# Kernel optimization log

Hardware: AMD Instinct MI355X
Metric: run time of the kernel (lower is better)

## Reference

```python
import jax, jax.numpy as jnp
import numpy as np

NUM_HEADS = 12
H = W = 64            # spatial grid (SAM ViT-B global attention)
DIM = 768
HEAD_DIM = DIM // NUM_HEADS


def setup_inputs() -> dict:
    key = jax.random.key(0)
    ks = jax.random.split(key, 7)
    return {
        "x": jax.random.normal(ks[0], (1, H, W, DIM), dtype=jnp.float32),
        "qkv_w": jax.random.normal(ks[1], (3 * DIM, DIM), dtype=jnp.float32) * 0.02,
        "qkv_b": jax.random.normal(ks[2], (3 * DIM,), dtype=jnp.float32) * 0.02,
        "proj_w": jax.random.normal(ks[3], (DIM, DIM), dtype=jnp.float32) * 0.02,
        "proj_b": jax.random.normal(ks[4], (DIM,), dtype=jnp.float32) * 0.02,
        "rel_pos_h": jax.random.normal(ks[5], (2 * H - 1, HEAD_DIM), dtype=jnp.float32) * 0.02,
        "rel_pos_w": jax.random.normal(ks[6], (2 * W - 1, HEAD_DIM), dtype=jnp.float32) * 0.02,
    }


def _get_rel_pos(size: int, rel_pos: jnp.ndarray) -> jnp.ndarray:
    # q_size == k_size == size; rel_pos already has length 2*size-1 (no interp).
    coords = jnp.arange(size)[:, None] - jnp.arange(size)[None, :] + (size - 1)
    return rel_pos[coords]  # [size, size, head_dim]


def reference(x, qkv_w, qkv_b, proj_w, proj_b, rel_pos_h, rel_pos_w):
    B, h, w, C = x.shape
    nh, hd = NUM_HEADS, C // NUM_HEADS
    S = h * w
    scale = hd ** -0.5

    qkv = x.reshape(B, S, C) @ qkv_w.T + qkv_b            # [B, S, 3C]
    qkv = qkv.reshape(B, S, 3, nh, hd).transpose(2, 0, 3, 1, 4)
    qkv = qkv.reshape(3, B * nh, S, hd)
    q, k, v = qkv[0], qkv[1], qkv[2]                      # [B*nh, S, hd]

    attn = jnp.einsum('bqc,bkc->bqk', q * scale, k)       # [B*nh, S, S]

    Rh = _get_rel_pos(h, rel_pos_h)                       # [h, h, hd]
    Rw = _get_rel_pos(w, rel_pos_w)                       # [w, w, hd]
    r_q = q.reshape(B * nh, h, w, hd)
    rel_h = jnp.einsum('bhwc,hkc->bhwk', r_q, Rh)         # [B*nh, h, w, h]
    rel_w = jnp.einsum('bhwc,wkc->bhwk', r_q, Rw)         # [B*nh, h, w, w]
    attn = (attn.reshape(B * nh, h, w, h, w)
            + rel_h[:, :, :, :, None]
            + rel_w[:, :, :, None, :]).reshape(B * nh, S, S)

    attn = jax.nn.softmax(attn, axis=-1)
    out = jnp.einsum('bqk,bkc->bqc', attn, v)             # [B*nh, S, hd]
    out = out.reshape(B, nh, h, w, hd).transpose(0, 2, 3, 1, 4).reshape(B, h, w, C)
    return out @ proj_w.T + proj_b
```

## Files before the change

kernel.cpp:

```cpp
#include <hip/hip_runtime.h>


typedef __bf16 bf16;
typedef __bf16 bf16x8 __attribute__((ext_vector_type(8)));
typedef __bf16 bf16x4 __attribute__((ext_vector_type(4)));
typedef float f32x4 __attribute__((ext_vector_type(4)));
typedef float f32x16 __attribute__((ext_vector_type(16)));
typedef unsigned int u32;

__device__ __forceinline__ f32x4 mfma16(bf16x8 a, bf16x8 b, f32x4 c) {
  return __builtin_amdgcn_mfma_f32_16x16x32_bf16(a, b, c, 0, 0, 0);
}
__device__ __forceinline__ f32x16 mfma32(bf16x8 a, bf16x8 b, f32x16 c) {
  return __builtin_amdgcn_mfma_f32_32x32x16_bf16(a, b, c, 0, 0, 0);
}

typedef const __attribute__((address_space(1))) void* gas_ptr;
typedef __attribute__((address_space(3))) void* las_ptr;
__device__ __forceinline__ void gl_lds16(const void* g, void* l) {
  __builtin_amdgcn_global_load_lds((gas_ptr)g, (las_ptr)l, 16, 0, 0);
}

#if defined(__has_builtin)
#if __has_builtin(__builtin_amdgcn_permlane32_swap)
#define HAVE_PLSWAP 1
#endif
#endif
__device__ __forceinline__ void pswap_u(u32& a, u32& b) {
#ifdef HAVE_PLSWAP
  auto r = __builtin_amdgcn_permlane32_swap(a, b, false, false);
  a = r[0]; b = r[1];
#else
  const bool hi = (threadIdx.x & 32) != 0;
  u32 sa = (u32)__shfl_xor((int)a, 32, 64);
  u32 sb = (u32)__shfl_xor((int)b, 32, 64);
  u32 na = hi ? sb : a;
  u32 nb = hi ? b : sa;
  a = na; b = nb;
#endif
}
__device__ __forceinline__ void pswap_f(float& a, float& b) {
  u32 x = __float_as_uint(a), y = __float_as_uint(b);
  pswap_u(x, y);
  a = __uint_as_float(x); b = __uint_as_float(y);
}

#define L2E 1.4426950408889634f
#define SCK 0.18033688011112042f

__global__ __launch_bounds__(256) void cvt3(
    const float* __restrict__ a, bf16* __restrict__ oa,
    const float* __restrict__ b, bf16* __restrict__ ob,
    const float* __restrict__ c, bf16* __restrict__ oc) {
  int blk = blockIdx.x;
  const float* src;
  bf16* dst;
  int base;
  if (blk < 1536)       { src = a; dst = oa; base = blk; }
  else if (blk < 2400)  { src = b; dst = ob; base = blk - 1536; }
  else                  { src = c; dst = oc; base = blk - 2400; }
  int idx = (base * 256 + threadIdx.x) * 8;
  f32x4 x = *(const f32x4*)&src[idx];
  f32x4 y = *(const f32x4*)&src[idx + 4];
  bf16x8 o;
#pragma unroll
  for (int j = 0; j < 4; j++) { o[j] = (bf16)x[j]; o[j + 4] = (bf16)y[j]; }
  *(bf16x8*)&dst[idx] = o;
}

template <int MODE>
__global__ __launch_bounds__(256) void gemm128(
    const bf16* __restrict__ A, const bf16* __restrict__ B,
    const float* __restrict__ bias, int K, int N,
    bf16* __restrict__ q_s, bf16* __restrict__ k_f, bf16* __restrict__ v_f,
    float* __restrict__ outf) {
  __shared__ __align__(16) bf16 lA[128 * 64];
  __shared__ __align__(16) bf16 lB[128 * 64];
  const int tid = threadIdx.x;
  const int w = tid >> 6, l = tid & 63;
  const int nbx = gridDim.x;
  const int flat = blockIdx.y * nbx + blockIdx.x;
  const int nwg = nbx * gridDim.y;
  const int idx = (flat & 7) * (nwg >> 3) + (flat >> 3);
  const int n0 = (idx % nbx) * 128, m0 = (idx / nbx) * 128;

  f32x4 acc[4][4] = {};

  int rowc[4], sloc[4];
#pragma unroll
  for (int j = 0; j < 4; j++) {
    const int c = w * 4 + j;
    rowc[j] = c * 8 + (l >> 3);
    sloc[j] = (((l & 7) ^ (l >> 3) ^ c) & 7) * 8;
  }
  const int mw = (w & 1) * 64, nw = (w >> 1) * 64;

  for (int k0 = 0; k0 < K; k0 += 64) {
    __syncthreads();
#pragma unroll
    for (int j = 0; j < 4; j++) {
      gl_lds16(&A[(size_t)(m0 + rowc[j]) * K + k0 + sloc[j]],
               (char*)lA + (w * 4 + j) * 1024);
      gl_lds16(&B[(size_t)(n0 + rowc[j]) * K + k0 + sloc[j]],
               (char*)lB + (w * 4 + j) * 1024);
    }
    __syncthreads();
    bf16x8 af[2][4], bfr[2][4];
#pragma unroll
    for (int ks = 0; ks < 2; ks++)
#pragma unroll
      for (int i = 0; i < 4; i++) {
        const int rA = mw + i * 16 + (l & 15);
        const int rB = nw + i * 16 + (l & 15);
        const int slot = ks * 4 + (l >> 4);
        const int fA = ((rA ^ (rA >> 3)) & 7), fB = ((rB ^ (rB >> 3)) & 7);
        af[ks][i] = *(const bf16x8*)((const char*)lA + rA * 128 + ((slot ^ fA) & 7) * 16);
        bfr[ks][i] = *(const bf16x8*)((const char*)lB + rB * 128 + ((slot ^ fB) & 7) * 16);
      }
#pragma unroll
    for (int ks = 0; ks < 2; ks++)
#pragma unroll
      for (int mi = 0; mi < 4; mi++)
#pragma unroll
        for (int ni = 0; ni < 4; ni++)
          acc[mi][ni] = mfma16(af[ks][mi], bfr[ks][ni], acc[mi][ni]);
  }

  if (MODE == 0 && n0 >= 1536) {
    bf16* Lt = lA;
#pragma unroll 1
    for (int pass = 0; pass < 2; ++pass) {
      __syncthreads();
      if ((w >> 1) == pass) {
        char* R = (char*)Lt + (w & 1) * 8192;
#pragma unroll
        for (int ni = 0; ni < 4; ni++) {
          const float bv = bias[n0 + nw + ni * 16 + (l & 15)];
          const int nl = ni * 16 + (l & 15);
#pragma unroll
          for (int mi = 0; mi < 4; mi++)
#pragma unroll
            for (int i2 = 0; i2 < 2; i2++) {
              const int ml2 = (mi * 16 + (l >> 4) * 4 + i2 * 2) * 2;
              union { bf16 b[2]; u32 u; } pk;
              pk.b[0] = (bf16)(acc[mi][ni][i2 * 2] + bv);
              pk.b[1] = (bf16)(acc[mi][ni][i2 * 2 + 1] + bv);
              *(u32*)(R + nl * 128 + (ml2 ^ ((nl & 7) << 4))) = pk.u;
            }
        }
      }
      __syncthreads();
      if ((w >> 1) == pass) {
        const char* R = (const char*)Lt + (w & 1) * 8192;
#pragma unroll
        for (int r = 0; r < 8; r++) {
          const int nl = r * 8 + (l >> 3);
          const int pc = ((l & 7) * 16) ^ ((nl & 7) << 4);
          bf16x8 val = *(const bf16x8*)(R + nl * 128 + pc);
          const int n = n0 + pass * 64 + nl;
          const int head = (n - 1536) >> 6, hd = n & 63;
          const int mg = m0 + (w & 1) * 64 + (l & 7) * 8;
          const int t = mg >> 6, kh2 = (mg >> 5) & 1;
          const int st = (mg >> 4) & 1, hh = (mg >> 3) & 1;
          const size_t vidx =
              ((((((size_t)head * 64 + t) * 2 + kh2) * 2 + st) * 2 + hh) * 64 +
               hd) * 8;
          *(bf16x8*)&v_f[vidx] = val;
        }
      }
    }
    return;
  }

#pragma unroll
  for (int ni = 0; ni < 4; ni++) {
    const int n = n0 + nw + ni * 16 + (l & 15);
    const float bv = bias[n];
#pragma unroll
    for (int mi = 0; mi < 4; mi++) {
#pragma unroll
      for (int i = 0; i < 4; i++) {
        const int m = m0 + mw + mi * 16 + (l >> 4) * 4 + i;
        const float v = acc[mi][ni][i] + bv;
        if (MODE == 0) {
          const int which = n / 768, hn = n % 768;
          const int head = hn >> 6, hd = hn & 63;
          if (which == 0) {
            q_s[((size_t)head * 4096 + m) * 64 + hd] = (bf16)v;
          } else {
            const int t = m >> 6, kh2 = (m >> 5) & 1, r5 = m & 31;
            const int s = hd >> 4, h = (hd >> 3) & 1, j = hd & 7;
            const size_t kidx =
                ((((((size_t)head * 64 + t) * 2 + kh2) * 4 + s) * 2 + h) * 32 +
                 r5) * 8 + j;
            k_f[kidx] = (bf16)(v * SCK);
          }
        } else {
          outf[(size_t)m * N + n] = v;
        }
      }
    }
  }
}

__global__ __launch_bounds__(64) void rel_pos_w(
    const bf16* __restrict__ q_s, const float* __restrict__ table,
    float* __restrict__ out) {
  const int l = threadIdx.x;
  const int p = blockIdx.x, head = blockIdx.y;
  const size_t hbase = (size_t)head * 4096 * 64;

  f32x4 acc[4][4] = {};
#pragma unroll
  for (int ks = 0; ks < 2; ks++) {
    bf16x8 af[4], bfr[4];
#pragma unroll
    for (int mi = 0; mi < 4; mi++) {
      const int row = mi * 16 + (l & 15);
      const int s = row * 64 + p;
      af[mi] = *(const bf16x8*)&q_s[hbase + (size_t)s * 64 + ks * 32 + (l >> 4) * 8];
    }
#pragma unroll
    for (int ni = 0; ni < 4; ni++) {
      const int col = ni * 16 + (l & 15);
      const float* tp = &table[(size_t)(p - col + 63) * 64 + ks * 32 + (l >> 4) * 8];
      f32x4 t0 = *(const f32x4*)tp;
      f32x4 t1 = *(const f32x4*)(tp + 4);
      bf16x8 bb;
#pragma unroll
      for (int j = 0; j < 4; j++) { bb[j] = (bf16)t0[j]; bb[j + 4] = (bf16)t1[j]; }
      bfr[ni] = bb;
    }
#pragma unroll
    for (int mi = 0; mi < 4; mi++)
#pragma unroll
      for (int ni = 0; ni < 4; ni++)
        acc[mi][ni] = mfma16(af[mi], bfr[ni], acc[mi][ni]);
  }
#pragma unroll
  for (int mi = 0; mi < 4; mi++)
#pragma unroll
    for (int ni = 0; ni < 4; ni++)
#pragma unroll
      for (int i = 0; i < 4; i++) {
        const int row = mi * 16 + (l >> 4) * 4 + i;
        const int col = ni * 16 + (l & 15);
        const int sq = row * 64 + p;
        out[hbase + (size_t)sq * 64 + col] = acc[mi][ni][i];
      }
}

__global__ __launch_bounds__(256, 3) void flash_attn(
    const bf16* __restrict__ q_s, const bf16* __restrict__ k_f,
    const bf16* __restrict__ v_f, const float* __restrict__ rph,
    const float* __restrict__ bias_w, bf16* __restrict__ attn_out) {
  __shared__ __align__(16) char smem[16896];
  float* lBH = (float*)smem;

  const int tid = threadIdx.x;
  const int w = tid >> 6, l = tid & 63;
  const int r5 = l & 31, h = l >> 5;
  const int qg = w & 1, kh2 = w >> 1;
  const int f = blockIdx.x;
  const int g = (f & 7) * 96 + (f >> 3);
  const int head = g >> 6, qh = g & 63;
  const size_t hbase = (size_t)head << 18;
  const int qloc = qg * 32 + r5;
  const size_t sq = (size_t)qh * 64 + qloc;

  {
    const int q16 = l & 15, g4 = l >> 4;
    const size_t sq16 = (size_t)qh * 64 + w * 16 + q16;
    bf16x8 qf16[2];
    qf16[0] = *(const bf16x8*)&q_s[hbase + sq16 * 64 + g4 * 8];
    qf16[1] = *(const bf16x8*)&q_s[hbase + sq16 * 64 + 32 + g4 * 8];
    f32x4 abh[4] = {};
#pragma unroll
    for (int ks = 0; ks < 2; ks++)
#pragma unroll
      for (int ni = 0; ni < 4; ni++) {
        const int kh = ni * 16 + q16;
        const float* tp = &rph[(size_t)(qh + 63 - kh) * 64 + ks * 32 + g4 * 8];
        f32x4 t0 = *(const f32x4*)tp;
        f32x4 t1 = *(const f32x4*)(tp + 4);
        bf16x8 rf;
#pragma unroll
        for (int j = 0; j < 4; j++) { rf[j] = (bf16)t0[j]; rf[j + 4] = (bf16)t1[j]; }
        abh[ni] = mfma16(rf, qf16[ks], abh[ni]);
      }
#pragma unroll
    for (int ni = 0; ni < 4; ni++)
#pragma unroll
      for (int i = 0; i < 4; i++)
        lBH[(w * 16 + q16) * 65 + ni * 16 + g4 * 4 + i] = abh[ni][i] * L2E;
  }

  bf16x8 qv[4];
#pragma unroll
  for (int s = 0; s < 4; s++)
    qv[s] = *(const bf16x8*)&q_s[hbase + sq * 64 + s * 16 + h * 8];

  f32x16 c2v;
#pragma unroll
  for (int G = 0; G < 4; G++) {
    f32x4 cv = *(const f32x4*)&bias_w[hbase + sq * 64 + kh2 * 32 + G * 8 + h * 4];
#pragma unroll
    for (int i = 0; i < 4; i++) c2v[G * 4 + i] = cv[i] * L2E;
  }

  const bf16* kp = k_f + hbase + kh2 * 2048 + h * 256 + r5 * 8;
  const bf16* vp = v_f + hbase + kh2 * 2048 + h * 512 + r5 * 8;
  const float* lbhp = lBH + qloc * 65;

  f32x16 o[2] = {};
  float mrun = -1e30f, lrun = 0.f;

  __syncthreads();

  for (int t = 0; t < 64; t++) {
    f32x16 sacc = c2v;
    __builtin_amdgcn_s_setprio(1);
#pragma unroll
    for (int s = 0; s < 4; s++) {
      bf16x8 kf = *(const bf16x8*)((const char*)kp + s * 1024);
      sacc = mfma32(kf, qv[s], sacc);
    }
    __builtin_amdgcn_s_setprio(0);

    float pm = fmaxf(
        fmaxf(fmaxf(fmaxf(sacc[0], sacc[1]), sacc[2]),
              fmaxf(fmaxf(sacc[3], sacc[4]), sacc[5])),
        fmaxf(fmaxf(fmaxf(sacc[6], sacc[7]), fmaxf(sacc[8], sacc[9])),
              fmaxf(fmaxf(sacc[10], fmaxf(sacc[11], sacc[12])),
                    fmaxf(sacc[13], fmaxf(sacc[14], sacc[15])))));
    { float t2 = pm; pswap_f(t2, pm); pm = fmaxf(t2, pm); }
    const float bh2 = lbhp[t];
    const float rmf = pm + bh2;

    if (!__all(rmf - mrun <= 8.f)) {
      const float mn = fmaxf(mrun, rmf);
      const float al = __builtin_amdgcn_exp2f(mrun - mn);
      mrun = mn;
      lrun *= al;
      o[0] *= al;
      o[1] *= al;
    }

    const float d = bh2 - mrun;
    float rs = 0.f;
    u32 w8[8];
#pragma unroll
    for (int j = 0; j < 8; j++) {
      float e0 = __builtin_amdgcn_exp2f(sacc[2 * j] + d);
      float e1 = __builtin_amdgcn_exp2f(sacc[2 * j + 1] + d);
      rs += e0 + e1;
      union { bf16 b[2]; u32 u; } cvu;
      cvu.b[0] = (bf16)e0;
      cvu.b[1] = (bf16)e1;
      w8[j] = cvu.u;
    }
    { float t2 = rs; pswap_f(t2, rs); rs = t2 + rs; }
    lrun += rs;

#pragma unroll
    for (int st = 0; st < 2; st++) {
      union { u32 u[4]; bf16x8 v; } pf;
      u32 a0 = w8[4 * st], b0 = w8[4 * st + 2];
      u32 a1 = w8[4 * st + 1], b1 = w8[4 * st + 3];
      pswap_u(a0, b0);
      pswap_u(a1, b1);
      pf.u[0] = a0; pf.u[1] = a1; pf.u[2] = b0; pf.u[3] = b1;
      __builtin_amdgcn_s_setprio(1);
#pragma unroll
      for (int T = 0; T < 2; T++) {
        bf16x8 vf = *(const bf16x8*)((const char*)vp + st * 2048 + T * 512);
        o[T] = mfma32(vf, pf.v, o[T]);
      }
      __builtin_amdgcn_s_setprio(0);
    }

    kp += 4096;
    vp += 4096;
  }

  __syncthreads();

  float* MM = (float*)smem;
  float* ML = (float*)(smem + 256);
  float* MO = (float*)(smem + 512);
  if (w >= 2) {
    if (h == 0) { MM[qg * 32 + r5] = mrun; ML[qg * 32 + r5] = lrun; }
#pragma unroll
    for (int T = 0; T < 2; T++)
#pragma unroll
      for (int G = 0; G < 4; G++) {
        f32x4 ov;
#pragma unroll
        for (int i = 0; i < 4; i++) ov[i] = o[T][4 * G + i];
        *(f32x4*)&MO[qg * 2048 + r5 * 64 + T * 32 + G * 8 + h * 4] = ov;
      }
  }
  __syncthreads();
  if (w < 2) {
    const float mp = MM[qg * 32 + r5], lp = ML[qg * 32 + r5];
    const float mT = fmaxf(mrun, mp);
    const float a = __builtin_amdgcn_exp2f(mrun - mT);
    const float b = __builtin_amdgcn_exp2f(mp - mT);
    const float inv = 1.f / (lrun * a + lp * b);
#pragma unroll
    for (int T = 0; T < 2; T++)
#pragma unroll
      for (int G = 0; G < 4; G++) {
        f32x4 po = *(const f32x4*)&MO[qg * 2048 + r5 * 64 + T * 32 + G * 8 + h * 4];
        bf16x4 ob;
#pragma unroll
        for (int i = 0; i < 4; i++)
          ob[i] = (bf16)((o[T][4 * G + i] * a + po[i] * b) * inv);
        *(bf16x4*)&attn_out[sq * 768 + head * 64 + T * 32 + G * 8 + h * 4] = ob;
      }
  }
}

extern "C" void kernel_launch(void* const* d_in, const int* in_sizes, int n_in,
                              void* d_out, int out_size, void* d_ws, size_t ws_size,
                              hipStream_t stream) {
  const float* x      = (const float*)d_in[0];
  const float* qkv_w  = (const float*)d_in[1];
  const float* qkv_b  = (const float*)d_in[2];
  const float* proj_w = (const float*)d_in[3];
  const float* proj_b = (const float*)d_in[4];
  const float* rph    = (const float*)d_in[5];
  const float* rpw    = (const float*)d_in[6];

  char* ws = (char*)d_ws;
  bf16*  xb    = (bf16*)(ws);
  bf16*  wqkv  = (bf16*)(ws + 6291456);
  bf16*  wproj = (bf16*)(ws + 9830400);
  bf16*  q_s   = (bf16*)(ws + 11010048);
  bf16*  k_f   = (bf16*)(ws + 17301504);
  bf16*  v_f   = (bf16*)(ws + 23592960);
  bf16*  attno = (bf16*)(ws + 29884416);
  float* bwv   = (float*)(ws + 36175872);

  cvt3<<<2688, 256, 0, stream>>>(x, xb, qkv_w, wqkv, proj_w, wproj);

  gemm128<0><<<dim3(18, 32), 256, 0, stream>>>(xb, wqkv, qkv_b, 768, 2304,
                                               q_s, k_f, v_f, nullptr);

  rel_pos_w<<<dim3(64, 12), 64, 0, stream>>>(q_s, rpw, bwv);

  flash_attn<<<768, 256, 0, stream>>>(q_s, k_f, v_f, rph, bwv, attno);

  gemm128<1><<<dim3(6, 32), 256, 0, stream>>>(attno, wproj, proj_b, 768, 768,
                                              nullptr, nullptr, nullptr,
                                              (float*)d_out);
}
```

Measured before the change: 257.3 us.

## Software-pipeline K/V register loads in flash attention and pre-convert rel-pos tables

The flash attention main loop is unrolled by two and double-buffers the K fragments in registers, loading the next tile's K and the current V before the current tile's compute so global latency overlaps the MFMA and softmax work. Separately, the rel_pos_h and rel_pos_w tables are converted to bf16 once in the cvt kernel, so the rel-pos and attention kernels read bf16 directly instead of loading fp32 and converting per use. The extra live registers from double buffering may raise register pressure under the 3-blocks-per-SM launch bound and risk spills.

```diff
diff --git a/kernel.cpp b/kernel.cpp
--- a/kernel.cpp
+++ b/kernel.cpp
@@ -51,15 +51,20 @@
 __global__ __launch_bounds__(256) void cvt3(
     const float* __restrict__ a, bf16* __restrict__ oa,
     const float* __restrict__ b, bf16* __restrict__ ob,
-    const float* __restrict__ c, bf16* __restrict__ oc) {
+    const float* __restrict__ c, bf16* __restrict__ oc,
+    const float* __restrict__ t1, bf16* __restrict__ ot1,
+    const float* __restrict__ t2, bf16* __restrict__ ot2) {
   int blk = blockIdx.x;
   const float* src;
   bf16* dst;
-  int base;
-  if (blk < 1536)       { src = a; dst = oa; base = blk; }
-  else if (blk < 2400)  { src = b; dst = ob; base = blk - 1536; }
-  else                  { src = c; dst = oc; base = blk - 2400; }
+  int base, lim;
+  if (blk < 1536)       { src = a;  dst = oa;  base = blk;        lim = 3145728; }
+  else if (blk < 2400)  { src = b;  dst = ob;  base = blk - 1536; lim = 1769472; }
+  else if (blk < 2688)  { src = c;  dst = oc;  base = blk - 2400; lim = 589824; }
+  else if (blk < 2692)  { src = t1; dst = ot1; base = blk - 2688; lim = 8128; }
+  else                  { src = t2; dst = ot2; base = blk - 2692; lim = 8128; }
   int idx = (base * 256 + threadIdx.x) * 8;
+  if (idx >= lim) return;
   f32x4 x = *(const f32x4*)&src[idx];
   f32x4 y = *(const f32x4*)&src[idx + 4];
   bf16x8 o;
@@ -204,7 +209,7 @@
 }
 
 __global__ __launch_bounds__(64) void rel_pos_w(
-    const bf16* __restrict__ q_s, const float* __restrict__ table,
+    const bf16* __restrict__ q_s, const bf16* __restrict__ rpw_b,
     float* __restrict__ out) {
   const int l = threadIdx.x;
   const int p = blockIdx.x, head = blockIdx.y;
@@ -223,13 +228,8 @@
 #pragma unroll
     for (int ni = 0; ni < 4; ni++) {
       const int col = ni * 16 + (l & 15);
-      const float* tp = &table[(size_t)(p - col + 63) * 64 + ks * 32 + (l >> 4) * 8];
-      f32x4 t0 = *(const f32x4*)tp;
-      f32x4 t1 = *(const f32x4*)(tp + 4);
-      bf16x8 bb;
-#pragma unroll
-      for (int j = 0; j < 4; j++) { bb[j] = (bf16)t0[j]; bb[j + 4] = (bf16)t1[j]; }
-      bfr[ni] = bb;
+      bfr[ni] = *(const bf16x8*)&rpw_b[(size_t)(p - col + 63) * 64 + ks * 32 +
+                                       (l >> 4) * 8];
     }
 #pragma unroll
     for (int mi = 0; mi < 4; mi++)
@@ -252,7 +252,7 @@
 
 __global__ __launch_bounds__(256, 3) void flash_attn(
     const bf16* __restrict__ q_s, const bf16* __restrict__ k_f,
-    const bf16* __restrict__ v_f, const float* __restrict__ rph,
+    const bf16* __restrict__ v_f, const bf16* __restrict__ rph_b,
     const float* __restrict__ bias_w, bf16* __restrict__ attn_out) {
   __shared__ __align__(16) char smem[16896];
   float* lBH = (float*)smem;
@@ -280,12 +280,8 @@
 #pragma unroll
       for (int ni = 0; ni < 4; ni++) {
         const int kh = ni * 16 + q16;
-        const float* tp = &rph[(size_t)(qh + 63 - kh) * 64 + ks * 32 + g4 * 8];
-        f32x4 t0 = *(const f32x4*)tp;
-        f32x4 t1 = *(const f32x4*)(tp + 4);
-        bf16x8 rf;
-#pragma unroll
-        for (int j = 0; j < 4; j++) { rf[j] = (bf16)t0[j]; rf[j + 4] = (bf16)t1[j]; }
+        bf16x8 rf = *(const bf16x8*)&rph_b[(size_t)(qh + 63 - kh) * 64 +
+                                           ks * 32 + g4 * 8];
         abh[ni] = mfma16(rf, qf16[ks], abh[ni]);
       }
 #pragma unroll
@@ -315,73 +311,96 @@
   f32x16 o[2] = {};
   float mrun = -1e30f, lrun = 0.f;
 
+  bf16x8 kA0 = *(const bf16x8*)(kp);
+  bf16x8 kA1 = *(const bf16x8*)(kp + 512);
+  bf16x8 kA2 = *(const bf16x8*)(kp + 1024);
+  bf16x8 kA3 = *(const bf16x8*)(kp + 1536);
+  kp += 4096;
+  bf16x8 kB0, kB1, kB2, kB3, v0, v1, v2, v3;
+
+#define COMP(K0, K1, K2, K3, t)                                              \
+  do {                                                                       \
+    f32x16 sacc = c2v;                                                       \
+    __builtin_amdgcn_s_setprio(1);                                           \
+    sacc = mfma32(K0, qv[0], sacc);                                          \
+    sacc = mfma32(K1, qv[1], sacc);                                          \
+    sacc = mfma32(K2, qv[2], sacc);                                          \
+    sacc = mfma32(K3, qv[3], sacc);                                          \
+    __builtin_amdgcn_s_setprio(0);                                           \
+    float pm = fmaxf(                                                        \
+        fmaxf(fmaxf(fmaxf(sacc[0], sacc[1]), sacc[2]),                       \
+              fmaxf(fmaxf(sacc[3], sacc[4]), sacc[5])),                      \
+        fmaxf(fmaxf(fmaxf(sacc[6], sacc[7]), fmaxf(sacc[8], sacc[9])),       \
+              fmaxf(fmaxf(sacc[10], fmaxf(sacc[11], sacc[12])),              \
+                    fmaxf(sacc[13], fmaxf(sacc[14], sacc[15])))));           \
+    { float t2_ = pm; pswap_f(t2_, pm); pm = fmaxf(t2_, pm); }               \
+    const float bh2 = lbhp[(t)];                                             \
+    const float rmf = pm + bh2;                                              \
+    if (!__all(rmf - mrun <= 8.f)) {                                         \
+      const float mn = fmaxf(mrun, rmf);                                     \
+      const float al = __builtin_amdgcn_exp2f(mrun - mn);                    \
+      mrun = mn;                                                             \
+      lrun *= al;                                                            \
+      o[0] *= al;                                                            \
+      o[1] *= al;                                                            \
+    }                                                                        \
+    const float d = bh2 - mrun;                                              \
+    float rs = 0.f;                                                          \
+    u32 w8[8];                                                               \
+    _Pragma("unroll")                                                        \
+    for (int j = 0; j < 8; j++) {                                            \
+      float e0 = __builtin_amdgcn_exp2f(sacc[2 * j] + d);                    \
+      float e1 = __builtin_amdgcn_exp2f(sacc[2 * j + 1] + d);                \
+      rs += e0 + e1;                                                         \
+      union { bf16 b[2]; u32 u; } cvu;                                       \
+      cvu.b[0] = (bf16)e0;                                                   \
+      cvu.b[1] = (bf16)e1;                                                   \
+      w8[j] = cvu.u;                                                         \
+    }                                                                        \
+    { float t2_ = rs; pswap_f(t2_, rs); rs = t2_ + rs; }                     \
+    lrun += rs;                                                              \
+    _Pragma("unroll")                                                        \
+    for (int st = 0; st < 2; st++) {                                         \
+      union { u32 u[4]; bf16x8 v; } pf;                                      \
+      u32 a0 = w8[4 * st], b0 = w8[4 * st + 2];                              \
+      u32 a1 = w8[4 * st + 1], b1 = w8[4 * st + 3];                          \
+      pswap_u(a0, b0);                                                       \
+      pswap_u(a1, b1);                                                       \
+      pf.u[0] = a0; pf.u[1] = a1; pf.u[2] = b0; pf.u[3] = b1;                \
+      __builtin_amdgcn_s_setprio(1);                                         \
+      o[0] = mfma32(st ? v2 : v0, pf.v, o[0]);                               \
+      o[1] = mfma32(st ? v3 : v1, pf.v, o[1]);                               \
+      __builtin_amdgcn_s_setprio(0);                                         \
+    }                                                                        \
+  } while (0)
+
   __syncthreads();
 
-  for (int t = 0; t < 64; t++) {
-    f32x16 sacc = c2v;
-    __builtin_amdgcn_s_setprio(1);
-#pragma unroll
-    for (int s = 0; s < 4; s++) {
-      bf16x8 kf = *(const bf16x8*)((const char*)kp + s * 1024);
-      sacc = mfma32(kf, qv[s], sacc);
-    }
-    __builtin_amdgcn_s_setprio(0);
-
-    float pm = fmaxf(
-        fmaxf(fmaxf(fmaxf(sacc[0], sacc[1]), sacc[2]),
-              fmaxf(fmaxf(sacc[3], sacc[4]), sacc[5])),
-        fmaxf(fmaxf(fmaxf(sacc[6], sacc[7]), fmaxf(sacc[8], sacc[9])),
-              fmaxf(fmaxf(sacc[10], fmaxf(sacc[11], sacc[12])),
-                    fmaxf(sacc[13], fmaxf(sacc[14], sacc[15])))));
-    { float t2 = pm; pswap_f(t2, pm); pm = fmaxf(t2, pm); }
-    const float bh2 = lbhp[t];
-    const float rmf = pm + bh2;
-
-    if (!__all(rmf - mrun <= 8.f)) {
-      const float mn = fmaxf(mrun, rmf);
-      const float al = __builtin_amdgcn_exp2f(mrun - mn);
-      mrun = mn;
-      lrun *= al;
-      o[0] *= al;
-      o[1] *= al;
-    }
-
-    const float d = bh2 - mrun;
-    float rs = 0.f;
-    u32 w8[8];
-#pragma unroll
-    for (int j = 0; j < 8; j++) {
-      float e0 = __builtin_amdgcn_exp2f(sacc[2 * j] + d);
-      float e1 = __builtin_amdgcn_exp2f(sacc[2 * j + 1] + d);
-      rs += e0 + e1;
-      union { bf16 b[2]; u32 u; } cvu;
-      cvu.b[0] = (bf16)e0;
-      cvu.b[1] = (bf16)e1;
-      w8[j] = cvu.u;
-    }
-    { float t2 = rs; pswap_f(t2, rs); rs = t2 + rs; }
-    lrun += rs;
-
-#pragma unroll
-    for (int st = 0; st < 2; st++) {
-      union { u32 u[4]; bf16x8 v; } pf;
-      u32 a0 = w8[4 * st], b0 = w8[4 * st + 2];
-      u32 a1 = w8[4 * st + 1], b1 = w8[4 * st + 3];
-      pswap_u(a0, b0);
-      pswap_u(a1, b1);
-      pf.u[0] = a0; pf.u[1] = a1; pf.u[2] = b0; pf.u[3] = b1;
-      __builtin_amdgcn_s_setprio(1);
-#pragma unroll
-      for (int T = 0; T < 2; T++) {
-        bf16x8 vf = *(const bf16x8*)((const char*)vp + st * 2048 + T * 512);
-        o[T] = mfma32(vf, pf.v, o[T]);
-      }
-      __builtin_amdgcn_s_setprio(0);
-    }
-
+  for (int t = 0; t < 64; t += 2) {
+    v0 = *(const bf16x8*)(vp);
+    v1 = *(const bf16x8*)(vp + 256);
+    v2 = *(const bf16x8*)(vp + 1024);
+    v3 = *(const bf16x8*)(vp + 1280);
+    kB0 = *(const bf16x8*)(kp);
+    kB1 = *(const bf16x8*)(kp + 512);
+    kB2 = *(const bf16x8*)(kp + 1024);
+    kB3 = *(const bf16x8*)(kp + 1536);
     kp += 4096;
     vp += 4096;
-  }
+    COMP(kA0, kA1, kA2, kA3, t);
+    v0 = *(const bf16x8*)(vp);
+    v1 = *(const bf16x8*)(vp + 256);
+    v2 = *(const bf16x8*)(vp + 1024);
+    v3 = *(const bf16x8*)(vp + 1280);
+    kA0 = *(const bf16x8*)(kp);
+    kA1 = *(const bf16x8*)(kp + 512);
+    kA2 = *(const bf16x8*)(kp + 1024);
+    kA3 = *(const bf16x8*)(kp + 1536);
+    kp += 4096;
+    vp += 4096;
+    COMP(kB0, kB1, kB2, kB3, t + 1);
+  }
+#undef COMP
 
   __syncthreads();
 
@@ -441,15 +460,18 @@
   bf16*  v_f   = (bf16*)(ws + 23592960);
   bf16*  attno = (bf16*)(ws + 29884416);
   float* bwv   = (float*)(ws + 36175872);
-
-  cvt3<<<2688, 256, 0, stream>>>(x, xb, qkv_w, wqkv, proj_w, wproj);
+  bf16*  rph_b = (bf16*)(ws + 48758784);
+  bf16*  rpw_b = (bf16*)(ws + 48775040);
+
+  cvt3<<<2696, 256, 0, stream>>>(x, xb, qkv_w, wqkv, proj_w, wproj,
+                                 rph, rph_b, rpw, rpw_b);
 
   gemm128<0><<<dim3(18, 32), 256, 0, stream>>>(xb, wqkv, qkv_b, 768, 2304,
                                                q_s, k_f, v_f, nullptr);
 
-  rel_pos_w<<<dim3(64, 12), 64, 0, stream>>>(q_s, rpw, bwv);
-
-  flash_attn<<<768, 256, 0, stream>>>(q_s, k_f, v_f, rph, bwv, attno);
+  rel_pos_w<<<dim3(64, 12), 64, 0, stream>>>(q_s, rpw_b, bwv);
+
+  flash_attn<<<768, 256, 0, stream>>>(q_s, k_f, v_f, rph_b, bwv, attno);
 
   gemm128<1><<<dim3(6, 32), 256, 0, stream>>>(attno, wproj, proj_b, 768, 768,
                                               nullptr, nullptr, nullptr,
```

New measurement: 247.8 us. -3.7%, faster.

## Split flash attention key loop across 8 waves and pre-convert rel-pos tables

Applied to the files above, without the earlier changes.

The flash attention kernel now runs 512 threads per block, so each query group's 64 key tiles are split four ways (two kh2 halves times two interleaved tiles) instead of two. The per-block merge becomes a 4-way log-sum-exp combine through larger shared memory. K and V fragments are also loaded at the top of each iteration ahead of the MFMAs to hide latency. The rel-pos tables are converted to bf16 once in the cvt kernel and rel_pos_w packs 4 positions per block. The cost is more LDS (51KB), a heavier reduction, and possibly lower occupancy.

```diff
diff --git a/kernel.cpp b/kernel.cpp
--- a/kernel.cpp
+++ b/kernel.cpp
@@ -51,15 +51,20 @@
 __global__ __launch_bounds__(256) void cvt3(
     const float* __restrict__ a, bf16* __restrict__ oa,
     const float* __restrict__ b, bf16* __restrict__ ob,
-    const float* __restrict__ c, bf16* __restrict__ oc) {
+    const float* __restrict__ c, bf16* __restrict__ oc,
+    const float* __restrict__ t1, bf16* __restrict__ ot1,
+    const float* __restrict__ t2, bf16* __restrict__ ot2) {
   int blk = blockIdx.x;
   const float* src;
   bf16* dst;
-  int base;
-  if (blk < 1536)       { src = a; dst = oa; base = blk; }
-  else if (blk < 2400)  { src = b; dst = ob; base = blk - 1536; }
-  else                  { src = c; dst = oc; base = blk - 2400; }
+  int base, lim;
+  if (blk < 1536)       { src = a;  dst = oa;  base = blk;        lim = 3145728; }
+  else if (blk < 2400)  { src = b;  dst = ob;  base = blk - 1536; lim = 1769472; }
+  else if (blk < 2688)  { src = c;  dst = oc;  base = blk - 2400; lim = 589824; }
+  else if (blk < 2692)  { src = t1; dst = ot1; base = blk - 2688; lim = 8128; }
+  else                  { src = t2; dst = ot2; base = blk - 2692; lim = 8128; }
   int idx = (base * 256 + threadIdx.x) * 8;
+  if (idx >= lim) return;
   f32x4 x = *(const f32x4*)&src[idx];
   f32x4 y = *(const f32x4*)&src[idx + 4];
   bf16x8 o;
@@ -203,11 +208,12 @@
   }
 }
 
-__global__ __launch_bounds__(64) void rel_pos_w(
-    const bf16* __restrict__ q_s, const float* __restrict__ table,
+__global__ __launch_bounds__(256) void rel_pos_w(
+    const bf16* __restrict__ q_s, const bf16* __restrict__ rpw_b,
     float* __restrict__ out) {
-  const int l = threadIdx.x;
-  const int p = blockIdx.x, head = blockIdx.y;
+  const int l = threadIdx.x & 63;
+  const int p = blockIdx.x * 4 + (threadIdx.x >> 6);
+  const int head = blockIdx.y;
   const size_t hbase = (size_t)head * 4096 * 64;
 
   f32x4 acc[4][4] = {};
@@ -223,13 +229,8 @@
 #pragma unroll
     for (int ni = 0; ni < 4; ni++) {
       const int col = ni * 16 + (l & 15);
-      const float* tp = &table[(size_t)(p - col + 63) * 64 + ks * 32 + (l >> 4) * 8];
-      f32x4 t0 = *(const f32x4*)tp;
-      f32x4 t1 = *(const f32x4*)(tp + 4);
-      bf16x8 bb;
-#pragma unroll
-      for (int j = 0; j < 4; j++) { bb[j] = (bf16)t0[j]; bb[j + 4] = (bf16)t1[j]; }
-      bfr[ni] = bb;
+      bfr[ni] = *(const bf16x8*)&rpw_b[(size_t)(p - col + 63) * 64 + ks * 32 +
+                                       (l >> 4) * 8];
     }
 #pragma unroll
     for (int mi = 0; mi < 4; mi++)
@@ -250,17 +251,17 @@
       }
 }
 
-__global__ __launch_bounds__(256, 3) void flash_attn(
+__global__ __launch_bounds__(512, 4) void flash_attn(
     const bf16* __restrict__ q_s, const bf16* __restrict__ k_f,
-    const bf16* __restrict__ v_f, const float* __restrict__ rph,
+    const bf16* __restrict__ v_f, const bf16* __restrict__ rph_b,
     const float* __restrict__ bias_w, bf16* __restrict__ attn_out) {
-  __shared__ __align__(16) char smem[16896];
+  __shared__ __align__(16) char smem[51200];
   float* lBH = (float*)smem;
 
   const int tid = threadIdx.x;
   const int w = tid >> 6, l = tid & 63;
   const int r5 = l & 31, h = l >> 5;
-  const int qg = w & 1, kh2 = w >> 1;
+  const int kh2 = w & 1, tp = (w >> 1) & 1, qg = w >> 2;
   const int f = blockIdx.x;
   const int g = (f & 7) * 96 + (f >> 3);
   const int head = g >> 6, qh = g & 63;
@@ -268,7 +269,7 @@
   const int qloc = qg * 32 + r5;
   const size_t sq = (size_t)qh * 64 + qloc;
 
-  {
+  if (w < 4) {
     const int q16 = l & 15, g4 = l >> 4;
     const size_t sq16 = (size_t)qh * 64 + w * 16 + q16;
     bf16x8 qf16[2];
@@ -280,12 +281,8 @@
 #pragma unroll
       for (int ni = 0; ni < 4; ni++) {
         const int kh = ni * 16 + q16;
-        const float* tp = &rph[(size_t)(qh + 63 - kh) * 64 + ks * 32 + g4 * 8];
-        f32x4 t0 = *(const f32x4*)tp;
-        f32x4 t1 = *(const f32x4*)(tp + 4);
-        bf16x8 rf;
-#pragma unroll
-        for (int j = 0; j < 4; j++) { rf[j] = (bf16)t0[j]; rf[j + 4] = (bf16)t1[j]; }
+        bf16x8 rf = *(const bf16x8*)&rph_b[(size_t)(qh + 63 - kh) * 64 +
+                                           ks * 32 + g4 * 8];
         abh[ni] = mfma16(rf, qf16[ks], abh[ni]);
       }
 #pragma unroll
@@ -308,23 +305,33 @@
     for (int i = 0; i < 4; i++) c2v[G * 4 + i] = cv[i] * L2E;
   }
 
-  const bf16* kp = k_f + hbase + kh2 * 2048 + h * 256 + r5 * 8;
-  const bf16* vp = v_f + hbase + kh2 * 2048 + h * 512 + r5 * 8;
-  const float* lbhp = lBH + qloc * 65;
+  const bf16* kp = k_f + hbase + tp * 4096 + kh2 * 2048 + h * 256 + r5 * 8;
+  const bf16* vp = v_f + hbase + tp * 4096 + kh2 * 2048 + h * 512 + r5 * 8;
+  const float* lbhp = lBH + qloc * 65 + tp;
 
   f32x16 o[2] = {};
   float mrun = -1e30f, lrun = 0.f;
 
   __syncthreads();
 
-  for (int t = 0; t < 64; t++) {
+  for (int i = 0; i < 32; i++) {
+    bf16x8 k0 = *(const bf16x8*)(kp);
+    bf16x8 k1 = *(const bf16x8*)(kp + 512);
+    bf16x8 k2 = *(const bf16x8*)(kp + 1024);
+    bf16x8 k3 = *(const bf16x8*)(kp + 1536);
+    bf16x8 v0 = *(const bf16x8*)(vp);
+    bf16x8 v1 = *(const bf16x8*)(vp + 256);
+    bf16x8 v2 = *(const bf16x8*)(vp + 1024);
+    bf16x8 v3 = *(const bf16x8*)(vp + 1280);
+    kp += 8192;
+    vp += 8192;
+
     f32x16 sacc = c2v;
     __builtin_amdgcn_s_setprio(1);
-#pragma unroll
-    for (int s = 0; s < 4; s++) {
-      bf16x8 kf = *(const bf16x8*)((const char*)kp + s * 1024);
-      sacc = mfma32(kf, qv[s], sacc);
-    }
+    sacc = mfma32(k0, qv[0], sacc);
+    sacc = mfma32(k1, qv[1], sacc);
+    sacc = mfma32(k2, qv[2], sacc);
+    sacc = mfma32(k3, qv[3], sacc);
     __builtin_amdgcn_s_setprio(0);
 
     float pm = fmaxf(
@@ -334,7 +341,7 @@
               fmaxf(fmaxf(sacc[10], fmaxf(sacc[11], sacc[12])),
                     fmaxf(sacc[13], fmaxf(sacc[14], sacc[15])))));
     { float t2 = pm; pswap_f(t2, pm); pm = fmaxf(t2, pm); }
-    const float bh2 = lbhp[t];
+    const float bh2 = lbhp[2 * i];
     const float rmf = pm + bh2;
 
     if (!__all(rmf - mrun <= 8.f)) {
@@ -371,25 +378,23 @@
       pswap_u(a1, b1);
       pf.u[0] = a0; pf.u[1] = a1; pf.u[2] = b0; pf.u[3] = b1;
       __builtin_amdgcn_s_setprio(1);
-#pragma unroll
-      for (int T = 0; T < 2; T++) {
-        bf16x8 vf = *(const bf16x8*)((const char*)vp + st * 2048 + T * 512);
-        o[T] = mfma32(vf, pf.v, o[T]);
-      }
+      o[0] = mfma32(st ? v2 : v0, pf.v, o[0]);
+      o[1] = mfma32(st ? v3 : v1, pf.v, o[1]);
       __builtin_amdgcn_s_setprio(0);
     }
-
-    kp += 4096;
-    vp += 4096;
   }
 
   __syncthreads();
 
   float* MM = (float*)smem;
-  float* ML = (float*)(smem + 256);
-  float* MO = (float*)(smem + 512);
-  if (w >= 2) {
-    if (h == 0) { MM[qg * 32 + r5] = mrun; ML[qg * 32 + r5] = lrun; }
+  float* ML = (float*)(smem + 1024);
+  float* MO = (float*)(smem + 2048);
+  const int slot = (w & 3) - 1;
+  if ((w & 3) != 0) {
+    if (h == 0) {
+      MM[(qg * 3 + slot) * 32 + r5] = mrun;
+      ML[(qg * 3 + slot) * 32 + r5] = lrun;
+    }
 #pragma unroll
     for (int T = 0; T < 2; T++)
 #pragma unroll
@@ -397,25 +402,32 @@
         f32x4 ov;
 #pragma unroll
         for (int i = 0; i < 4; i++) ov[i] = o[T][4 * G + i];
-        *(f32x4*)&MO[qg * 2048 + r5 * 64 + T * 32 + G * 8 + h * 4] = ov;
+        *(f32x4*)&MO[((qg * 3 + slot) * 32 + r5) * 64 + T * 32 + G * 8 + h * 4] = ov;
       }
   }
   __syncthreads();
-  if (w < 2) {
-    const float mp = MM[qg * 32 + r5], lp = ML[qg * 32 + r5];
-    const float mT = fmaxf(mrun, mp);
+  if ((w & 3) == 0) {
+    float mp0 = MM[(qg * 3 + 0) * 32 + r5], lp0 = ML[(qg * 3 + 0) * 32 + r5];
+    float mp1 = MM[(qg * 3 + 1) * 32 + r5], lp1 = ML[(qg * 3 + 1) * 32 + r5];
+    float mp2 = MM[(qg * 3 + 2) * 32 + r5], lp2 = ML[(qg * 3 + 2) * 32 + r5];
+    const float mT = fmaxf(fmaxf(mrun, mp0), fmaxf(mp1, mp2));
     const float a = __builtin_amdgcn_exp2f(mrun - mT);
-    const float b = __builtin_amdgcn_exp2f(mp - mT);
-    const float inv = 1.f / (lrun * a + lp * b);
+    const float b0 = __builtin_amdgcn_exp2f(mp0 - mT);
+    const float b1 = __builtin_amdgcn_exp2f(mp1 - mT);
+    const float b2 = __builtin_amdgcn_exp2f(mp2 - mT);
+    const float inv = 1.f / (lrun * a + lp0 * b0 + lp1 * b1 + lp2 * b2);
 #pragma unroll
     for (int T = 0; T < 2; T++)
 #pragma unroll
       for (int G = 0; G < 4; G++) {
-        f32x4 po = *(const f32x4*)&MO[qg * 2048 + r5 * 64 + T * 32 + G * 8 + h * 4];
+        f32x4 p0 = *(const f32x4*)&MO[((qg * 3 + 0) * 32 + r5) * 64 + T * 32 + G * 8 + h * 4];
+        f32x4 p1 = *(const f32x4*)&MO[((qg * 3 + 1) * 32 + r5) * 64 + T * 32 + G * 8 + h * 4];
+        f32x4 p2 = *(const f32x4*)&MO[((qg * 3 + 2) * 32 + r5) * 64 + T * 32 + G * 8 + h * 4];
         bf16x4 ob;
 #pragma unroll
         for (int i = 0; i < 4; i++)
-          ob[i] = (bf16)((o[T][4 * G + i] * a + po[i] * b) * inv);
+          ob[i] = (bf16)((o[T][4 * G + i] * a + p0[i] * b0 + p1[i] * b1 +
+                          p2[i] * b2) * inv);
         *(bf16x4*)&attn_out[sq * 768 + head * 64 + T * 32 + G * 8 + h * 4] = ob;
       }
   }
@@ -441,15 +453,18 @@
   bf16*  v_f   = (bf16*)(ws + 23592960);
   bf16*  attno = (bf16*)(ws + 29884416);
   float* bwv   = (float*)(ws + 36175872);
-
-  cvt3<<<2688, 256, 0, stream>>>(x, xb, qkv_w, wqkv, proj_w, wproj);
+  bf16*  rph_b = (bf16*)(ws + 48758784);
+  bf16*  rpw_b = (bf16*)(ws + 48775040);
+
+  cvt3<<<2696, 256, 0, stream>>>(x, xb, qkv_w, wqkv, proj_w, wproj,
+                                 rph, rph_b, rpw, rpw_b);
 
   gemm128<0><<<dim3(18, 32), 256, 0, stream>>>(xb, wqkv, qkv_b, 768, 2304,
                                                q_s, k_f, v_f, nullptr);
 
-  rel_pos_w<<<dim3(64, 12), 64, 0, stream>>>(q_s, rpw, bwv);
-
-  flash_attn<<<768, 256, 0, stream>>>(q_s, k_f, v_f, rph, bwv, attno);
+  rel_pos_w<<<dim3(16, 12), 256, 0, stream>>>(q_s, rpw_b, bwv);
+
+  flash_attn<<<768, 512, 0, stream>>>(q_s, k_f, v_f, rph_b, bwv, attno);
 
   gemm128<1><<<dim3(6, 32), 256, 0, stream>>>(attno, wproj, proj_b, 768, 768,
                                               nullptr, nullptr, nullptr,
```

Result: slower. 603.7 us (+134.6%).
